# Kernel tuning notes

Measured on AMD Instinct MI355X. Metric: run time of the kernel, lower is better.

## Reference

```python
import jax, jax.numpy as jnp
import numpy as np
from jax import lax

B, T, N, H, NC = 2, 8, 512, 64, 10
NEG = -1e9
LN_EPS = 1e-5


def _gatv2(x, mask, Wl, Wr, att, b):
    # GATv2Conv (PyG semantics, eval mode): e_ij = att . leaky_relu(Wr x_i + Wl x_j),
    # softmax over source nodes j with self-loops, out_i = sum_j alpha_ij * (Wl x_j).
    # x: (B, N, Fin); mask: (N, N) bool adjacency incl. self-loops; att: (heads, C).
    heads, C = att.shape
    Bn, Nn, _ = x.shape
    xl = (x @ Wl).reshape(Bn, Nn, heads, C)  # source transform
    xr = (x @ Wr).reshape(Bn, Nn, heads, C)  # target transform
    s = jax.nn.leaky_relu(xr[:, :, None] + xl[:, None, :], 0.2)  # (B, Ni, Nj, h, C)
    e = jnp.einsum('bijhc,hc->bijh', s, att)
    e = jnp.where(mask[None, :, :, None], e, NEG)
    alpha = jax.nn.softmax(e, axis=2)  # softmax over neighbors j
    out = jnp.einsum('bijh,bjhc->bihc', alpha, xl)
    return out.reshape(Bn, Nn, heads * C) + b


def _gru_layer(x, Wih, Whh, bih, bhh):
    # torch nn.GRU single layer, batch_first; x: (B, T, Hin)
    h0 = jnp.zeros((x.shape[0], Whh.shape[0]), x.dtype)
    def step(h, xt):
        gi = xt @ Wih + bih
        gh = h @ Whh + bhh
        ir, iz, inn = jnp.split(gi, 3, axis=-1)
        hr, hz, hn = jnp.split(gh, 3, axis=-1)
        r = jax.nn.sigmoid(ir + hr)
        z = jax.nn.sigmoid(iz + hz)
        n = jnp.tanh(inn + r * hn)
        hnew = (1.0 - z) * n + z * h
        return hnew, hnew
    _, ys = lax.scan(step, h0, jnp.swapaxes(x, 0, 1))
    return jnp.swapaxes(ys, 0, 1)


def setup_inputs() -> dict:
    key = jax.random.key(0)
    ks = jax.random.split(key, 20)
    def rn(i, shape, s=0.1):
        return jax.random.normal(ks[i], shape, jnp.float32) * s
    x_seq = jax.random.normal(ks[0], (B, T, N, 1), jnp.float32)
    a = jax.random.uniform(ks[1], (N, N))
    up = jnp.triu((a > 0.95).astype(jnp.float32), 1)
    static_adj = up + up.T  # sparse symmetric 0/1 static graph
    dyn_W = jax.random.normal(ks[2], (N, N), jnp.float32)
    reg_lambda = jnp.array([0.05], jnp.float32)
    return {
        'x_seq': x_seq, 'static_adj': static_adj, 'dyn_W': dyn_W, 'reg_lambda': reg_lambda,
        'g1_Wl': rn(3, (1, H)), 'g1_Wr': rn(4, (1, H)), 'g1_att': rn(5, (4, H // 4)), 'g1_b': jnp.zeros(H),
        'g2_Wl': rn(6, (H, H)), 'g2_Wr': rn(7, (H, H)), 'g2_att': rn(8, (1, H)), 'g2_b': jnp.zeros(H),
        'gru_Wih0': rn(9, (H, 3 * H)), 'gru_Whh0': rn(10, (H, 3 * H)), 'gru_bih0': jnp.zeros(3 * H), 'gru_bhh0': jnp.zeros(3 * H),
        'gru_Wih1': rn(11, (H, 3 * H)), 'gru_Whh1': rn(12, (H, 3 * H)), 'gru_bih1': jnp.zeros(3 * H), 'gru_bhh1': jnp.zeros(3 * H),
        'attn_W': rn(13, (H, 1)), 'attn_b': jnp.zeros(1),
        'cls_W1': rn(14, (H, H)), 'cls_b1': jnp.zeros(H), 'ln_g': jnp.ones(H), 'ln_b': jnp.zeros(H),
        'cls_W2': rn(15, (H, NC)), 'cls_b2': jnp.zeros(NC),
    }


def reference(x_seq, static_adj, dyn_W, reg_lambda,
              g1_Wl, g1_Wr, g1_att, g1_b, g2_Wl, g2_Wr, g2_att, g2_b,
              gru_Wih0, gru_Whh0, gru_bih0, gru_bhh0,
              gru_Wih1, gru_Whh1, gru_bih1, gru_bhh1,
              attn_W, attn_b, cls_W1, cls_b1, ln_g, ln_b, cls_W2, cls_b2):
    Bn, Tn, Nn, _ = x_seq.shape
    lam = jnp.maximum(reg_lambda[0], 0.01)
    t = jnp.arange(Tn, dtype=x_seq.dtype)
    gts = jnp.exp(-lam * t)  # gating values per timestep
    dyn = jax.nn.relu(dyn_W + dyn_W.T)
    fused = gts[:, None, None] * static_adj + (1.0 - gts)[:, None, None] * dyn  # (T, N, N)
    masks = (fused > 0) | jnp.eye(Nn, dtype=bool)[None]  # edge set + self-loops

    def step(carry, inp):
        xt, mask = inp  # xt: (B, N, 1)
        h = jax.nn.elu(_gatv2(xt, mask, g1_Wl, g1_Wr, g1_att, g1_b))
        h = jax.nn.elu(_gatv2(h, mask, g2_Wl, g2_Wr, g2_att, g2_b))
        return carry, h.mean(axis=1)  # (B, H) graph readout

    _, reps = lax.scan(step, 0.0, (jnp.swapaxes(x_seq, 0, 1), masks))
    h_seq = jnp.swapaxes(reps, 0, 1)  # (B, T, H)

    gru_out = _gru_layer(h_seq, gru_Wih0, gru_Whh0, gru_bih0, gru_bhh0)
    gru_out = _gru_layer(gru_out, gru_Wih1, gru_Whh1, gru_bih1, gru_bhh1)

    att_scores = jax.nn.softmax((gru_out @ attn_W + attn_b)[..., 0], axis=1)  # (B, T)
    final = jnp.einsum('bt,bth->bh', att_scores, gru_out)

    z = final @ cls_W1 + cls_b1
    mu = jnp.mean(z, axis=-1, keepdims=True)
    var = jnp.var(z, axis=-1, keepdims=True)
    z = (z - mu) / jnp.sqrt(var + LN_EPS) * ln_g + ln_b
    z = jax.nn.gelu(z, approximate=False)
    logits = z @ cls_W2 + cls_b2
    return logits, gts, att_scores
```

## Files before the change

### kernel.cpp

```cpp
#include <hip/hip_runtime.h>
#include <math.h>

#define BB 2
#define TT 8
#define NN 512
#define HH 64
#define NC 10

typedef unsigned char uchar;

__device__ __forceinline__ float elu1(float v){ return v > 0.f ? v : expm1f(v); }
__device__ __forceinline__ float sigm(float v){ return 1.f/(1.f+expf(-v)); }

__global__ __launch_bounds__(256) void k_mask(
    const float* __restrict__ dW, const float* __restrict__ sadj,
    uchar* __restrict__ M0, uchar* __restrict__ M1,
    float* __restrict__ hseq,
    const float* __restrict__ att1, const float* __restrict__ Wr1,
    const float* __restrict__ Wl1, float* __restrict__ AB,
    const float* __restrict__ Whh0, const float* __restrict__ Whh1,
    float4* __restrict__ WT4)
{
    __shared__ float tr[64][65];
    int bx = blockIdx.x, by = blockIdx.y;
    int tid = threadIdx.x;
    if (blockIdx.z == 1){
        int idx = (by*8 + bx)*256 + tid;
        if (idx < 2*4096){
            int m = idx >> 12, r = idx & 4095;
            int k = r >> 6, gg = r & 63;
            const float* W = m ? Whh1 : Whh0;
            float4 o;
            o.x = W[k*192 + gg];
            o.y = W[k*192 + 64 + gg];
            o.z = W[k*192 + 128 + gg];
            o.w = 0.f;
            WT4[(size_t)m*4096 + r] = o;
        }
        return;
    }
    int i0 = by*64, j0 = bx*64;
    #pragma unroll
    for (int q = 0; q < 4; ++q){
        int r = (tid >> 4) + 16*q, c4 = tid & 15;
        float4 v = *(const float4*)&dW[(size_t)(j0+r)*NN + i0 + 4*c4];
        tr[r][4*c4+0] = v.x; tr[r][4*c4+1] = v.y;
        tr[r][4*c4+2] = v.z; tr[r][4*c4+3] = v.w;
    }
    __syncthreads();
    #pragma unroll
    for (int q = 0; q < 4; ++q){
        int row = (tid >> 4) + 16*q, c4 = tid & 15;
        int i = i0 + row, j = j0 + 4*c4;
        float4 d  = *(const float4*)&dW[(size_t)i*NN + j];
        float4 sa = *(const float4*)&sadj[(size_t)i*NN + j];
        uchar4 m0, m1;
        float dd0 = d.x + tr[4*c4+0][row];
        float dd1 = d.y + tr[4*c4+1][row];
        float dd2 = d.z + tr[4*c4+2][row];
        float dd3 = d.w + tr[4*c4+3][row];
        m0.x = (sa.x > 0.f) || (i == j+0);
        m0.y = (sa.y > 0.f) || (i == j+1);
        m0.z = (sa.z > 0.f) || (i == j+2);
        m0.w = (sa.w > 0.f) || (i == j+3);
        m1.x = m0.x || (dd0 > 0.f);
        m1.y = m0.y || (dd1 > 0.f);
        m1.z = m0.z || (dd2 > 0.f);
        m1.w = m0.w || (dd3 > 0.f);
        *(uchar4*)&M0[(size_t)i*NN + j] = m0;
        *(uchar4*)&M1[(size_t)i*NN + j] = m1;
    }
    int flat = (by*8 + bx)*256 + tid;
    if (flat < BB*TT*HH) hseq[flat] = 0.f;
    if (bx == 0 && by == 0 && tid < 8){
        int h = tid & 3;
        const float* W = (tid < 4) ? Wr1 : Wl1;
        float s = 0.f;
        for (int c = 0; c < 16; ++c) s += att1[h*16+c]*W[h*16+c];
        AB[tid] = s;
    }
}

__global__ __launch_bounds__(256) void k_gat1f(
    const float* __restrict__ x_seq, const uchar* __restrict__ M0,
    const uchar* __restrict__ M1,
    const float* __restrict__ Wl, const float* __restrict__ Wr,
    const float* __restrict__ att, const float* __restrict__ bias,
    const float* __restrict__ AB,
    const float* __restrict__ Wl2, const float* __restrict__ Wr2,
    const float* __restrict__ att2,
    float* __restrict__ xl2, float* __restrict__ xr2,
    float* __restrict__ ui, float* __restrict__ vj)
{
    __shared__ float x_s[NN];
    __shared__ float S_s[4][4];
    __shared__ float h_s[4][HH];
    __shared__ float Wl2_s[64*64];
    __shared__ float Wr2_s[64*64];
    int bt = blockIdx.y; int t = bt % TT;
    int i0 = blockIdx.x * 4;
    int tid = threadIdx.x;
    int il = tid >> 6, jl = tid & 63;
    int i = i0 + il;
    const uchar* M = t ? M1 : M0;
    ((float2*)x_s)[tid] = ((const float2*)(x_seq + bt*NN))[tid];
    #pragma unroll
    for (int q = 0; q < 4; ++q){
        int idx = q*256 + tid;
        ((float4*)Wl2_s)[idx] = ((const float4*)Wl2)[idx];
        ((float4*)Wr2_s)[idx] = ((const float4*)Wr2)[idx];
    }
    __syncthreads();
    float xi = x_s[i];
    const uchar* Mrow = M + (size_t)i*NN;
    float xj[8], msk[8];
    #pragma unroll
    for (int jj = 0; jj < 8; ++jj){
        int j = jj*64 + jl;
        xj[jj] = x_s[j];
        msk[jj] = Mrow[j] ? 1.f : 0.f;
    }
    float sw[4] = {0,0,0,0}, swx[4] = {0,0,0,0};
    for (int h = 0; h < 4; ++h){
        float acc[8] = {0,0,0,0,0,0,0,0};
        #pragma unroll
        for (int c = 0; c < 16; ++c){
            int hc = h*16 + c;
            float wl = Wl[hc];
            float q  = 0.4f * att[hc];
            float pr = xi * Wr[hc];
            #pragma unroll
            for (int jj = 0; jj < 8; ++jj){
                float s = fmaf(xj[jj], wl, pr);
                acc[jj] = fmaf(q, fabsf(s), acc[jj]);
            }
        }
        float lin = 0.6f * xi * AB[h];
        float al6 = 0.6f * AB[4+h];
        #pragma unroll
        for (int jj = 0; jj < 8; ++jj){
            float e = acc[jj] + fmaf(al6, xj[jj], lin);
            float w = msk[jj] * __expf(e);
            sw[h] += w;
            swx[h] = fmaf(w, xj[jj], swx[h]);
        }
    }
    #pragma unroll
    for (int off = 32; off; off >>= 1){
        #pragma unroll
        for (int h = 0; h < 4; ++h){
            sw[h]  += __shfl_down(sw[h],  off);
            swx[h] += __shfl_down(swx[h], off);
        }
    }
    if (jl == 0){
        #pragma unroll
        for (int h = 0; h < 4; ++h) S_s[il][h] = swx[h] / sw[h];
    }
    __syncthreads();
    {
        int hc = tid & 63, row = tid >> 6;
        float v = S_s[row][hc >> 4] * Wl[hc] + bias[hc];
        h_s[row][hc] = elu1(v);
    }
    __syncthreads();
    {
        int c = tid & 63, row = tid >> 6;
        float al = 0.f, ar = 0.f;
        #pragma unroll 8
        for (int k = 0; k < 64; ++k){
            float hv = h_s[row][k];
            al = fmaf(hv, Wl2_s[k*64 + c], al);
            ar = fmaf(hv, Wr2_s[k*64 + c], ar);
        }
        size_t ridx = (size_t)(bt*NN + i0 + row);
        xl2[ridx*HH + c] = al;
        xr2[ridx*HH + c] = ar;
        float a2 = att2[c];
        float pu = a2 * ar, pv = a2 * al;
        #pragma unroll
        for (int off = 32; off; off >>= 1){
            pu += __shfl_down(pu, off);
            pv += __shfl_down(pv, off);
        }
        if (c == 0){ ui[ridx] = pu; vj[ridx] = pv; }
    }
}

__global__ __launch_bounds__(512) void k_gat2(
    const float* __restrict__ xl2, const float* __restrict__ xr2,
    const uchar* __restrict__ M0, const uchar* __restrict__ M1,
    const float* __restrict__ att, const float* __restrict__ ui,
    const float* __restrict__ vj, const float* __restrict__ bias,
    float* __restrict__ hseq)
{
    __shared__ float xl_s[256][68];
    __shared__ float wT_s[256][36];
    __shared__ float v_s[256];
    __shared__ float z_s[32];

    int bt = blockIdx.y, t = bt & 7;
    int i0 = blockIdx.x * 32;
    int base = bt * NN;
    int tid = threadIdx.x;
    const uchar* M = t ? M1 : M0;

    int ig = __builtin_amdgcn_readfirstlane(tid >> 6);
    int jg = tid & 63;
    int ln = jg;
    int ig2 = ln >> 3, cg2 = ln & 7;

    const float* xrp0 = xr2 + (size_t)(base + i0 + ig*4 + 0)*HH;
    const float* xrp1 = xr2 + (size_t)(base + i0 + ig*4 + 1)*HH;
    const float* xrp2 = xr2 + (size_t)(base + i0 + ig*4 + 2)*HH;
    const float* xrp3 = xr2 + (size_t)(base + i0 + ig*4 + 3)*HH;
    float u0 = 0.6f*ui[base + i0 + ig*4 + 0];
    float u1 = 0.6f*ui[base + i0 + ig*4 + 1];
    float u2 = 0.6f*ui[base + i0 + ig*4 + 2];
    float u3 = 0.6f*ui[base + i0 + ig*4 + 3];

    float zreg[4] = {0.f,0.f,0.f,0.f};
    float acc[4][8];
    #pragma unroll
    for (int a = 0; a < 4; ++a)
        #pragma unroll
        for (int r = 0; r < 8; ++r) acc[a][r] = 0.f;

    for (int tile = 0; tile < 2; ++tile){
        int j0 = tile * 256;
        __syncthreads();
        #pragma unroll
        for (int q = 0; q < 8; ++q){
            int idx = q*512 + tid;
            int row = idx >> 4, c4 = idx & 15;
            ((float4*)&xl_s[row][0])[c4] = ((const float4*)&xl2[(size_t)(base+j0+row)*HH])[c4];
        }
        if (tid < 256) v_s[tid] = vj[base + j0 + tid];
        __syncthreads();
        float e[4][4];
        #pragma unroll
        for (int jj = 0; jj < 4; ++jj){
            float vv = 0.6f * v_s[jj*64 + jg];
            e[0][jj] = u0 + vv; e[1][jj] = u1 + vv;
            e[2][jj] = u2 + vv; e[3][jj] = u3 + vv;
        }
        #pragma unroll 4
        for (int c4 = 0; c4 < 16; ++c4){
            float4 a4 = *(const float4*)&att[c4*4];
            float qk[4];
            qk[0] = 0.4f*a4.x; qk[1] = 0.4f*a4.y; qk[2] = 0.4f*a4.z; qk[3] = 0.4f*a4.w;
            float rr[4][4];
            *(float4*)rr[0] = *(const float4*)&xrp0[c4*4];
            *(float4*)rr[1] = *(const float4*)&xrp1[c4*4];
            *(float4*)rr[2] = *(const float4*)&xrp2[c4*4];
            *(float4*)rr[3] = *(const float4*)&xrp3[c4*4];
            float xlv[4][4];
            #pragma unroll
            for (int jj = 0; jj < 4; ++jj)
                *(float4*)xlv[jj] = ((const float4*)&xl_s[jj*64+jg][0])[c4];
            #pragma unroll
            for (int jj = 0; jj < 4; ++jj)
                #pragma unroll
                for (int k = 0; k < 4; ++k){
                    float xc = xlv[jj][k];
                    #pragma unroll
                    for (int ii = 0; ii < 4; ++ii)
                        e[ii][jj] = fmaf(qk[k], fabsf(rr[ii][k] + xc), e[ii][jj]);
                }
        }
        #pragma unroll
        for (int jj = 0; jj < 4; ++jj){
            int j = jj*64 + jg;
            const uchar* mp = &M[(size_t)(i0 + ig*4)*NN + j0 + j];
            float w0 = mp[0]      ? __expf(e[0][jj]) : 0.f;
            float w1 = mp[NN]     ? __expf(e[1][jj]) : 0.f;
            float w2 = mp[2*NN]   ? __expf(e[2][jj]) : 0.f;
            float w3 = mp[3*NN]   ? __expf(e[3][jj]) : 0.f;
            zreg[0] += w0; zreg[1] += w1; zreg[2] += w2; zreg[3] += w3;
            float4 wq; wq.x = w0; wq.y = w1; wq.z = w2; wq.w = w3;
            *(float4*)&wT_s[j][ig*4] = wq;
        }
        __syncthreads();
        #pragma unroll 4
        for (int jj = 0; jj < 32; ++jj){
            int j = ig*32 + jj;
            float w4[4], xa[8];
            *(float4*)w4      = *(const float4*)&wT_s[j][ig2*4];
            *(float4*)&xa[0]  = ((const float4*)&xl_s[j][0])[cg2*2+0];
            *(float4*)&xa[4]  = ((const float4*)&xl_s[j][0])[cg2*2+1];
            #pragma unroll
            for (int a = 0; a < 4; ++a)
                #pragma unroll
                for (int r = 0; r < 8; ++r)
                    acc[a][r] = fmaf(w4[a], xa[r], acc[a][r]);
        }
    }
    __syncthreads();
    #pragma unroll
    for (int off = 32; off; off >>= 1){
        #pragma unroll
        for (int ii = 0; ii < 4; ++ii) zreg[ii] += __shfl_down(zreg[ii], off);
    }
    if (jg == 0){
        #pragma unroll
        for (int ii = 0; ii < 4; ++ii) z_s[ig*4+ii] = zreg[ii];
    }
    float* scratch = &xl_s[0][0];
    if (ig > 0){
        #pragma unroll
        for (int a = 0; a < 4; ++a)
            #pragma unroll
            for (int r = 0; r < 8; ++r)
                scratch[(a*8+r)*448 + (ig-1)*64 + ln] = acc[a][r];
    }
    __syncthreads();
    if (ig == 0){
        float pm[8];
        #pragma unroll
        for (int r = 0; r < 8; ++r) pm[r] = 0.f;
        #pragma unroll
        for (int a = 0; a < 4; ++a){
            float rz = 1.f / z_s[ig2*4 + a];
            #pragma unroll
            for (int r = 0; r < 8; ++r){
                float s = acc[a][r];
                #pragma unroll
                for (int w = 0; w < 7; ++w)
                    s += scratch[(a*8+r)*448 + w*64 + ln];
                float h = elu1(s*rz + bias[cg2*8 + r]);
                pm[r] += h;
            }
        }
        #pragma unroll
        for (int off = 32; off >= 8; off >>= 1){
            #pragma unroll
            for (int r = 0; r < 8; ++r) pm[r] += __shfl_down(pm[r], off);
        }
        if (ig2 == 0){
            #pragma unroll
            for (int r = 0; r < 8; ++r)
                atomicAdd(&hseq[bt*HH + cg2*8 + r], pm[r] * (1.f/(float)NN));
        }
    }
}

__global__ __launch_bounds__(256, 1) void k_gru2(
    const float* __restrict__ hseq, const float* __restrict__ Wih0,
    const float* __restrict__ bih0, const float4* __restrict__ WT4,
    const float* __restrict__ bhh0, const float* __restrict__ Wih1,
    const float* __restrict__ bih1, const float* __restrict__ bhh1,
    const float* __restrict__ lamp, const float* __restrict__ attn_W,
    const float* __restrict__ attn_b, const float* __restrict__ W1,
    const float* __restrict__ b1, const float* __restrict__ ln_g,
    const float* __restrict__ ln_b, const float* __restrict__ W2,
    const float* __restrict__ b2, float* __restrict__ out)
{
    __shared__ float wih0_s[64*192];
    __shared__ float wih1_s[64*192];
    __shared__ float gi_s[BB*TT*192];
    __shared__ float hs_s[BB*TT*HH];
    __shared__ float y_s[BB*TT*HH];
    __shared__ float part_s[2][BB][2][3][HH];
    __shared__ float sc_s[BB][TT], at_s[BB][TT];
    __shared__ float fin_s[BB][HH], z_s[BB][HH], g_s[BB][HH];
    __shared__ float mu_s[BB], iv_s[BB];
    int tid = threadIdx.x;
    int wave = tid >> 6, ln = tid & 63;
    int b = wave >> 1, half = wave & 1;

    #pragma unroll
    for (int i = 0; i < 12; ++i){
        int idx = i*256 + tid;
        ((float4*)wih0_s)[idx] = ((const float4*)Wih0)[idx];
        ((float4*)wih1_s)[idx] = ((const float4*)Wih1)[idx];
    }
    float wx[32], wy[32], wz[32];
    #pragma unroll
    for (int k = 0; k < 32; ++k){
        float4 w4 = WT4[(half*32 + k)*64 + ln];
        wx[k] = w4.x; wy[k] = w4.y; wz[k] = w4.z;
    }
    ((float4*)hs_s)[tid] = ((const float4*)hseq)[tid];
    __syncthreads();
    #pragma unroll
    for (int o = 0; o < 3; ++o){
        int idx4 = o*256 + tid;
        int bt = idx4 / 48, q = idx4 % 48;
        float4 a4 = ((const float4*)bih0)[q];
        const float* hr = &hs_s[bt*HH];
        #pragma unroll 4
        for (int k = 0; k < HH; ++k){
            float hk = hr[k];
            float4 w4 = ((const float4*)&wih0_s[k*192])[q];
            a4.x = fmaf(hk, w4.x, a4.x);
            a4.y = fmaf(hk, w4.y, a4.y);
            a4.z = fmaf(hk, w4.z, a4.z);
            a4.w = fmaf(hk, w4.w, a4.w);
        }
        ((float4*)&gi_s[bt*192])[q] = a4;
    }
    __syncthreads();
    {
        float bhr = bhh0[ln], bhz = bhh0[64+ln], bhn = bhh0[128+ln];
        float h = 0.f;
        for (int t = 0; t < TT; ++t){
            float pr = 0.f, pz = 0.f, pn = 0.f;
            #pragma unroll
            for (int k = 0; k < 32; ++k){
                float hk = __shfl(h, half*32 + k);
                pr = fmaf(wx[k], hk, pr);
                pz = fmaf(wy[k], hk, pz);
                pn = fmaf(wz[k], hk, pn);
            }
            int pc = t & 1;
            part_s[pc][b][half][0][ln] = pr;
            part_s[pc][b][half][1][ln] = pz;
            part_s[pc][b][half][2][ln] = pn;
            __syncthreads();
            float ghr = pr + part_s[pc][b][1-half][0][ln] + bhr;
            float ghz = pz + part_s[pc][b][1-half][1][ln] + bhz;
            float ghn = pn + part_s[pc][b][1-half][2][ln] + bhn;
            const float* gi = &gi_s[(b*TT+t)*192];
            float r = sigm(gi[ln] + ghr);
            float z = sigm(gi[64+ln] + ghz);
            float n = tanhf(gi[128+ln] + r*ghn);
            h = (1.f - z)*n + z*h;
            if (half == 0) y_s[(b*TT+t)*HH + ln] = h;
        }
    }
    #pragma unroll
    for (int k = 0; k < 32; ++k){
        float4 w4 = WT4[4096 + (half*32 + k)*64 + ln];
        wx[k] = w4.x; wy[k] = w4.y; wz[k] = w4.z;
    }
    __syncthreads();
    #pragma unroll
    for (int o = 0; o < 3; ++o){
        int idx4 = o*256 + tid;
        int bt = idx4 / 48, q = idx4 % 48;
        float4 a4 = ((const float4*)bih1)[q];
        const float* yr = &y_s[bt*HH];
        #pragma unroll 4
        for (int k = 0; k < HH; ++k){
            float yk = yr[k];
            float4 w4 = ((const float4*)&wih1_s[k*192])[q];
            a4.x = fmaf(yk, w4.x, a4.x);
            a4.y = fmaf(yk, w4.y, a4.y);
            a4.z = fmaf(yk, w4.z, a4.z);
            a4.w = fmaf(yk, w4.w, a4.w);
        }
        ((float4*)&gi_s[bt*192])[q] = a4;
    }
    __syncthreads();
    {
        float bhr = bhh1[ln], bhz = bhh1[64+ln], bhn = bhh1[128+ln];
        float h = 0.f;
        for (int t = 0; t < TT; ++t){
            float pr = 0.f, pz = 0.f, pn = 0.f;
            #pragma unroll
            for (int k = 0; k < 32; ++k){
                float hk = __shfl(h, half*32 + k);
                pr = fmaf(wx[k], hk, pr);
                pz = fmaf(wy[k], hk, pz);
                pn = fmaf(wz[k], hk, pn);
            }
            int pc = t & 1;
            part_s[pc][b][half][0][ln] = pr;
            part_s[pc][b][half][1][ln] = pz;
            part_s[pc][b][half][2][ln] = pn;
            __syncthreads();
            float ghr = pr + part_s[pc][b][1-half][0][ln] + bhr;
            float ghz = pz + part_s[pc][b][1-half][1][ln] + bhz;
            float ghn = pn + part_s[pc][b][1-half][2][ln] + bhn;
            const float* gi = &gi_s[(b*TT+t)*192];
            float r = sigm(gi[ln] + ghr);
            float z = sigm(gi[64+ln] + ghz);
            float n = tanhf(gi[128+ln] + r*ghn);
            h = (1.f - z)*n + z*h;
            if (half == 0) y_s[(b*TT+t)*HH + ln] = h;
        }
    }
    __syncthreads();
    float lam = fmaxf(lamp[0], 0.01f);
    if (tid < TT) out[BB*NC + tid] = expf(-lam*(float)tid);
    if (tid < BB*TT){
        int bb = tid >> 3, t = tid & 7;
        float s = attn_b[0];
        const float* r = &y_s[(bb*TT+t)*HH];
        for (int h = 0; h < HH; ++h) s += r[h]*attn_W[h];
        sc_s[bb][t] = s;
    }
    __syncthreads();
    if (tid < BB){
        float mx = -INFINITY;
        for (int t = 0; t < TT; ++t) mx = fmaxf(mx, sc_s[tid][t]);
        float se = 0.f;
        for (int t = 0; t < TT; ++t){ float w = expf(sc_s[tid][t]-mx); at_s[tid][t] = w; se += w; }
        for (int t = 0; t < TT; ++t){
            at_s[tid][t] /= se;
            out[BB*NC + TT + tid*TT + t] = at_s[tid][t];
        }
    }
    __syncthreads();
    if (tid < BB*HH){
        int bb = tid >> 6, h = tid & 63;
        float a = 0.f;
        for (int t = 0; t < TT; ++t) a += at_s[bb][t]*y_s[(bb*TT+t)*HH + h];
        fin_s[bb][h] = a;
    }
    __syncthreads();
    if (tid < BB*HH){
        int bb = tid >> 6, h = tid & 63;
        float a = b1[h];
        for (int k = 0; k < HH; ++k) a += fin_s[bb][k]*W1[k*HH+h];
        z_s[bb][h] = a;
    }
    __syncthreads();
    if (tid < BB){
        float mu = 0.f;
        for (int h = 0; h < HH; ++h) mu += z_s[tid][h];
        mu *= (1.f/HH);
        float v = 0.f;
        for (int h = 0; h < HH; ++h){ float d = z_s[tid][h]-mu; v += d*d; }
        v *= (1.f/HH);
        mu_s[tid] = mu; iv_s[tid] = 1.f/sqrtf(v + 1e-5f);
    }
    __syncthreads();
    if (tid < BB*HH){
        int bb = tid >> 6, h = tid & 63;
        float zn = (z_s[bb][h]-mu_s[bb])*iv_s[bb]*ln_g[h] + ln_b[h];
        g_s[bb][h] = 0.5f*zn*(1.f + erff(zn*0.70710678118654752f));
    }
    __syncthreads();
    if (tid < BB*NC){
        int bb = tid / NC, c = tid % NC;
        float a = b2[c];
        for (int k = 0; k < HH; ++k) a += g_s[bb][k]*W2[k*NC+c];
        out[bb*NC + c] = a;
    }
}

extern "C" void kernel_launch(void* const* d_in, const int* in_sizes, int n_in,
                              void* d_out, int out_size, void* d_ws, size_t ws_size,
                              hipStream_t stream)
{
    const float* x_seq = (const float*)d_in[0];
    const float* sadj  = (const float*)d_in[1];
    const float* dynW  = (const float*)d_in[2];
    const float* lamp  = (const float*)d_in[3];
    const float* g1_Wl = (const float*)d_in[4];
    const float* g1_Wr = (const float*)d_in[5];
    const float* g1_att= (const float*)d_in[6];
    const float* g1_b  = (const float*)d_in[7];
    const float* g2_Wl = (const float*)d_in[8];
    const float* g2_Wr = (const float*)d_in[9];
    const float* g2_att= (const float*)d_in[10];
    const float* g2_b  = (const float*)d_in[11];
    const float* Wih0  = (const float*)d_in[12];
    const float* Whh0  = (const float*)d_in[13];
    const float* bih0  = (const float*)d_in[14];
    const float* bhh0  = (const float*)d_in[15];
    const float* Wih1  = (const float*)d_in[16];
    const float* Whh1  = (const float*)d_in[17];
    const float* bih1  = (const float*)d_in[18];
    const float* bhh1  = (const float*)d_in[19];
    const float* attnW = (const float*)d_in[20];
    const float* attnb = (const float*)d_in[21];
    const float* W1    = (const float*)d_in[22];
    const float* b1    = (const float*)d_in[23];
    const float* lng   = (const float*)d_in[24];
    const float* lnb   = (const float*)d_in[25];
    const float* W2    = (const float*)d_in[26];
    const float* b2    = (const float*)d_in[27];
    float* out = (float*)d_out;

    const int RWS = BB*TT*NN*HH;
    uchar* M0 = (uchar*)d_ws;
    uchar* M1 = M0 + (size_t)NN*NN;
    float* fb = (float*)(M1 + (size_t)NN*NN);
    float* AB   = fb;
    float* ui   = AB   + 16;
    float* vj   = ui   + BB*TT*NN;
    float* xl2  = vj   + BB*TT*NN;
    float* xr2  = xl2  + RWS;
    float* hseq = xr2  + RWS;
    float4* WT4 = (float4*)(hseq + BB*TT*HH);

    k_mask <<<dim3(8,8,2), 256, 0, stream>>>(dynW, sadj, M0, M1, hseq, g1_att, g1_Wr, g1_Wl, AB,
                                             Whh0, Whh1, WT4);
    k_gat1f<<<dim3(NN/4, BB*TT), 256, 0, stream>>>(x_seq, M0, M1, g1_Wl, g1_Wr, g1_att, g1_b, AB,
                                                   g2_Wl, g2_Wr, g2_att, xl2, xr2, ui, vj);
    k_gat2 <<<dim3(NN/32, BB*TT), 512, 0, stream>>>(xl2, xr2, M0, M1, g2_att, ui, vj, g2_b, hseq);
    k_gru2 <<<1, 256, 0, stream>>>(hseq, Wih0, bih0, WT4, bhh0, Wih1, bih1, bhh1,
                                   lamp, attnW, attnb, W1, b1, lng, lnb, W2, b2, out);
}
```

Before: 207.4 us.

## Make k_gat1f persistent-ish: 256 blocks of 512 threads looping over row tiles

Restructures the first GAT kernel from 2048 blocks of 256 threads handling 4 rows each into 256 blocks of 512 threads that loop over 4 sub-tiles of 8 rows. The goal is to amortise the per-block load of the two 64x64 layer-2 weight matrices into shared memory over 32 rows instead of 4. The cost is a serial loop with extra barriers, a reload of x_s on each iteration, and fewer blocks to fill the GPU (256 blocks on 256 CUs).

```diff
diff --git a/kernel.cpp b/kernel.cpp
--- a/kernel.cpp
+++ b/kernel.cpp
@@ -81,7 +81,7 @@
     }
 }
 
-__global__ __launch_bounds__(256) void k_gat1f(
+__global__ __launch_bounds__(512) void k_gat1f(
     const float* __restrict__ x_seq, const uchar* __restrict__ M0,
     const uchar* __restrict__ M1,
     const float* __restrict__ Wl, const float* __restrict__ Wr,
@@ -93,97 +93,102 @@
     float* __restrict__ ui, float* __restrict__ vj)
 {
     __shared__ float x_s[NN];
-    __shared__ float S_s[4][4];
-    __shared__ float h_s[4][HH];
+    __shared__ float S_s[8][4];
+    __shared__ float h_s[8][HH];
     __shared__ float Wl2_s[64*64];
     __shared__ float Wr2_s[64*64];
-    int bt = blockIdx.y; int t = bt % TT;
-    int i0 = blockIdx.x * 4;
     int tid = threadIdx.x;
-    int il = tid >> 6, jl = tid & 63;
-    int i = i0 + il;
-    const uchar* M = t ? M1 : M0;
-    ((float2*)x_s)[tid] = ((const float2*)(x_seq + bt*NN))[tid];
-    #pragma unroll
-    for (int q = 0; q < 4; ++q){
-        int idx = q*256 + tid;
+    #pragma unroll
+    for (int q = 0; q < 2; ++q){
+        int idx = q*512 + tid;
         ((float4*)Wl2_s)[idx] = ((const float4*)Wl2)[idx];
         ((float4*)Wr2_s)[idx] = ((const float4*)Wr2)[idx];
     }
-    __syncthreads();
-    float xi = x_s[i];
-    const uchar* Mrow = M + (size_t)i*NN;
-    float xj[8], msk[8];
-    #pragma unroll
-    for (int jj = 0; jj < 8; ++jj){
-        int j = jj*64 + jl;
-        xj[jj] = x_s[j];
-        msk[jj] = Mrow[j] ? 1.f : 0.f;
-    }
-    float sw[4] = {0,0,0,0}, swx[4] = {0,0,0,0};
-    for (int h = 0; h < 4; ++h){
-        float acc[8] = {0,0,0,0,0,0,0,0};
-        #pragma unroll
-        for (int c = 0; c < 16; ++c){
-            int hc = h*16 + c;
-            float wl = Wl[hc];
-            float q  = 0.4f * att[hc];
-            float pr = xi * Wr[hc];
+    int w = tid >> 6, jl = tid & 63;
+    for (int s = 0; s < 4; ++s){
+        int vb = blockIdx.x*4 + s;
+        int bt = vb >> 6, it = vb & 63;
+        int i0v = it*8;
+        int t = bt & 7;
+        const uchar* M = t ? M1 : M0;
+        __syncthreads();
+        x_s[tid] = x_seq[bt*NN + tid];
+        __syncthreads();
+        int i = i0v + w;
+        float xi = x_s[i];
+        const uchar* Mrow = M + (size_t)i*NN;
+        float xj[8], msk[8];
+        #pragma unroll
+        for (int jj = 0; jj < 8; ++jj){
+            int j = jj*64 + jl;
+            xj[jj] = x_s[j];
+            msk[jj] = Mrow[j] ? 1.f : 0.f;
+        }
+        float sw[4] = {0,0,0,0}, swx[4] = {0,0,0,0};
+        for (int h = 0; h < 4; ++h){
+            float acc[8] = {0,0,0,0,0,0,0,0};
+            #pragma unroll
+            for (int c = 0; c < 16; ++c){
+                int hc = h*16 + c;
+                float wl = Wl[hc];
+                float q  = 0.4f * att[hc];
+                float pr = xi * Wr[hc];
+                #pragma unroll
+                for (int jj = 0; jj < 8; ++jj){
+                    float sv = fmaf(xj[jj], wl, pr);
+                    acc[jj] = fmaf(q, fabsf(sv), acc[jj]);
+                }
+            }
+            float lin = 0.6f * xi * AB[h];
+            float al6 = 0.6f * AB[4+h];
             #pragma unroll
             for (int jj = 0; jj < 8; ++jj){
-                float s = fmaf(xj[jj], wl, pr);
-                acc[jj] = fmaf(q, fabsf(s), acc[jj]);
-            }
-        }
-        float lin = 0.6f * xi * AB[h];
-        float al6 = 0.6f * AB[4+h];
-        #pragma unroll
-        for (int jj = 0; jj < 8; ++jj){
-            float e = acc[jj] + fmaf(al6, xj[jj], lin);
-            float w = msk[jj] * __expf(e);
-            sw[h] += w;
-            swx[h] = fmaf(w, xj[jj], swx[h]);
-        }
-    }
-    #pragma unroll
-    for (int off = 32; off; off >>= 1){
-        #pragma unroll
-        for (int h = 0; h < 4; ++h){
-            sw[h]  += __shfl_down(sw[h],  off);
-            swx[h] += __shfl_down(swx[h], off);
-        }
-    }
-    if (jl == 0){
-        #pragma unroll
-        for (int h = 0; h < 4; ++h) S_s[il][h] = swx[h] / sw[h];
-    }
-    __syncthreads();
-    {
-        int hc = tid & 63, row = tid >> 6;
-        float v = S_s[row][hc >> 4] * Wl[hc] + bias[hc];
-        h_s[row][hc] = elu1(v);
-    }
-    __syncthreads();
-    {
-        int c = tid & 63, row = tid >> 6;
-        float al = 0.f, ar = 0.f;
-        #pragma unroll 8
-        for (int k = 0; k < 64; ++k){
-            float hv = h_s[row][k];
-            al = fmaf(hv, Wl2_s[k*64 + c], al);
-            ar = fmaf(hv, Wr2_s[k*64 + c], ar);
-        }
-        size_t ridx = (size_t)(bt*NN + i0 + row);
-        xl2[ridx*HH + c] = al;
-        xr2[ridx*HH + c] = ar;
-        float a2 = att2[c];
-        float pu = a2 * ar, pv = a2 * al;
+                float e = acc[jj] + fmaf(al6, xj[jj], lin);
+                float ww = msk[jj] * __expf(e);
+                sw[h] += ww;
+                swx[h] = fmaf(ww, xj[jj], swx[h]);
+            }
+        }
         #pragma unroll
         for (int off = 32; off; off >>= 1){
-            pu += __shfl_down(pu, off);
-            pv += __shfl_down(pv, off);
-        }
-        if (c == 0){ ui[ridx] = pu; vj[ridx] = pv; }
+            #pragma unroll
+            for (int h = 0; h < 4; ++h){
+                sw[h]  += __shfl_down(sw[h],  off);
+                swx[h] += __shfl_down(swx[h], off);
+            }
+        }
+        if (jl == 0){
+            #pragma unroll
+            for (int h = 0; h < 4; ++h) S_s[w][h] = swx[h] / sw[h];
+        }
+        __syncthreads();
+        {
+            int hc = tid & 63, row = tid >> 6;
+            float v = S_s[row][hc >> 4] * Wl[hc] + bias[hc];
+            h_s[row][hc] = elu1(v);
+        }
+        __syncthreads();
+        {
+            int c = tid & 63, row = tid >> 6;
+            float al = 0.f, ar = 0.f;
+            #pragma unroll 8
+            for (int k = 0; k < 64; ++k){
+                float hv = h_s[row][k];
+                al = fmaf(hv, Wl2_s[k*64 + c], al);
+                ar = fmaf(hv, Wr2_s[k*64 + c], ar);
+            }
+            size_t ridx = (size_t)(bt*NN + i0v + row);
+            xl2[ridx*HH + c] = al;
+            xr2[ridx*HH + c] = ar;
+            float a2 = att2[c];
+            float pu = a2 * ar, pv = a2 * al;
+            #pragma unroll
+            for (int off = 32; off; off >>= 1){
+                pu += __shfl_down(pu, off);
+                pv += __shfl_down(pv, off);
+            }
+            if (c == 0){ ui[ridx] = pu; vj[ridx] = pv; }
+        }
     }
 }
 
@@ -588,8 +593,8 @@
 
     k_mask <<<dim3(8,8,2), 256, 0, stream>>>(dynW, sadj, M0, M1, hseq, g1_att, g1_Wr, g1_Wl, AB,
                                              Whh0, Whh1, WT4);
-    k_gat1f<<<dim3(NN/4, BB*TT), 256, 0, stream>>>(x_seq, M0, M1, g1_Wl, g1_Wr, g1_att, g1_b, AB,
-                                                   g2_Wl, g2_Wr, g2_att, xl2, xr2, ui, vj);
+    k_gat1f<<<dim3(256), 512, 0, stream>>>(x_seq, M0, M1, g1_Wl, g1_Wr, g1_att, g1_b, AB,
+                                           g2_Wl, g2_Wr, g2_att, xl2, xr2, ui, vj);
     k_gat2 <<<dim3(NN/32, BB*TT), 512, 0, stream>>>(xl2, xr2, M0, M1, g2_att, ui, vj, g2_b, hseq);
     k_gru2 <<<1, 256, 0, stream>>>(hseq, Wih0, bih0, WT4, bhh0, Wih1, bih1, bhh1,
                                    lamp, attnW, attnb, W1, b1, lng, lnb, W2, b2, out);
```

After: 214.2 us. 3.3% more time.
